# Kernel optimization log

Hardware: AMD Instinct MI355X
Metric: run time of the kernel (lower is better)

## Reference

```python
import jax, jax.numpy as jnp
import numpy as np

QW, KW = 64, 128          # atom query / key window sizes
PAD = (KW - QW) // 2      # halo on each side of the key window
DEPTH, HEADS = 3, 4

def ln(x):
    m = jnp.mean(x, -1, keepdims=True)
    v = jnp.var(x, -1, keepdims=True)
    return (x - m) * jax.lax.rsqrt(v + 1e-5)

def q_windows(x):
    # x: (B, N, ...) -> (B, n, QW, ...); N assumed multiple of QW
    B, N = x.shape[0], x.shape[1]
    n = N // QW
    return x.reshape((B, n, QW) + x.shape[2:])

def k_windows(x):
    # x: (B, N, ...) -> (B, n, KW, ...) sliding key windows with zero halo padding
    B, N = x.shape[0], x.shape[1]
    n = N // QW
    pad_cfg = [(0, 0), (PAD, n * QW + PAD - N)] + [(0, 0)] * (x.ndim - 2)
    xp = jnp.pad(x, pad_cfg)
    idx = jnp.arange(n)[:, None] * QW + jnp.arange(KW)[None, :]
    return xp[:, idx]


def setup_inputs() -> dict:
    key = jax.random.key(0)
    ks = jax.random.split(key, 24)
    B, N, DS, DP, DT, NT = 2, 8192, 128, 16, 384, 1024
    w = lambda k, shp: (jax.random.normal(k, shp, jnp.float32) / np.sqrt(shp[-2])).astype(jnp.float32)
    inp = {
        'ref_pos': jax.random.normal(ks[0], (B, N, 3), jnp.float32),
        'ref_charge': jax.random.normal(ks[1], (B, N, 1), jnp.float32),
        'ref_mask': jnp.ones((B, N, 1), jnp.float32),
        'ref_element': jax.random.uniform(ks[2], (B, N, 128), jnp.float32),
        'ref_atom_name_chars': jax.random.uniform(ks[3], (B, N, 256), jnp.float32),
        'W_single': w(ks[4], (389, DS)),
        'W_pair': w(ks[5], (5, DP)),
        'W_outer': w(ks[6], (DS, 2 * DP)),
        'Wp_ff1': w(ks[7], (DP, 4 * DP)),
        'Wp_ff2': w(ks[8], (4 * DP, DP)),
        'Wq': w(ks[9], (DEPTH, DS, DS)),
        'Wk': w(ks[10], (DEPTH, DS, DS)),
        'Wv': w(ks[11], (DEPTH, DS, DS)),
        'Wo': w(ks[12], (DEPTH, DS, DS)),
        'Wb': w(ks[13], (DP, HEADS)),
        'Wff1': w(ks[14], (DEPTH, DS, 4 * DS)),
        'Wff2': w(ks[15], (DEPTH, 4 * DS, DS)),
        'W_out': w(ks[16], (DS, DT)),
        'ref_space_uid': jnp.sort(jax.random.randint(ks[17], (B, N), 0, NT), axis=-1),
        'atom_to_token_idx': jnp.sort(jax.random.randint(ks[18], (B, N), 0, NT), axis=-1),
        'n_tokens': NT,
    }
    return inp


def reference(ref_pos, ref_charge, ref_mask, ref_element, ref_atom_name_chars,
              W_single, W_pair, W_outer, Wp_ff1, Wp_ff2,
              Wq, Wk, Wv, Wo, Wb, Wff1, Wff2, W_out,
              ref_space_uid, atom_to_token_idx, n_tokens):
    B, N, _ = ref_pos.shape
    n = N // QW
    feats = jnp.concatenate([ref_pos, ref_charge, ref_mask, ref_element, ref_atom_name_chars], -1)
    s = feats @ W_single                                    # (B,N,DS) atom single repr

    # windowed pairwise geometric features
    pos_i, pos_j = q_windows(ref_pos), k_windows(ref_pos)   # (B,n,QW,3), (B,n,KW,3)
    uid_i, uid_j = q_windows(ref_space_uid), k_windows(ref_space_uid)
    dij = pos_i[:, :, :, None, :] - pos_j[:, :, None, :, :]  # (B,n,QW,KW,3)
    inv = 1.0 / (1.0 + jnp.sum(dij * dij, -1, keepdims=True))
    bij = (uid_i[:, :, :, None] == uid_j[:, :, None, :])
    pf = jnp.concatenate([dij, inv, bij[..., None].astype(dij.dtype)], -1)  # (...,5)
    pair = (pf @ W_pair) * bij[..., None].astype(dij.dtype)  # (B,n,QW,KW,DP)

    # pairwise outer-add from relu(single): Linear(DS->2*DP) split into i/j halves
    p = jax.nn.relu(s) @ W_outer
    DP = pair.shape[-1]
    pi, pj = p[..., :DP], p[..., DP:]
    pair = pair + q_windows(pi)[:, :, :, None, :] + k_windows(pj)[:, :, None, :, :]
    pair = pair + jax.nn.relu(ln(pair) @ Wp_ff1) @ Wp_ff2    # pair FF (residual)
    bias = jnp.einsum('bnqkc,ch->bnhqk', pair, Wb)           # attn pair bias

    # key validity mask for the halo-padded positions
    kidx = jnp.arange(n)[:, None] * QW + jnp.arange(KW)[None, :] - PAD
    kmask = jnp.where((kidx >= 0) & (kidx < N), 0.0, -1e9).astype(s.dtype)  # (n,KW)

    dh = s.shape[-1] // HEADS
    x = s
    for l in range(DEPTH):
        h = ln(x)
        q = q_windows(h @ Wq[l]).reshape(B, n, QW, HEADS, dh)
        k = k_windows(h @ Wk[l]).reshape(B, n, KW, HEADS, dh)
        v = k_windows(h @ Wv[l]).reshape(B, n, KW, HEADS, dh)
        logits = jnp.einsum('bnqhd,bnkhd->bnhqk', q, k) / np.sqrt(dh)
        logits = logits + bias + kmask[None, :, None, None, :]
        a = jax.nn.softmax(logits, -1)
        o = jnp.einsum('bnhqk,bnkhd->bnqhd', a, v).reshape(B, N, -1) @ Wo[l]
        x = x + o
        x = x + jax.nn.relu(ln(x) @ Wff1[l]) @ Wff2[l]

    tok = jax.nn.relu(x @ W_out)                             # (B,N,DT)

    def seg_mean(src, idx_):
        ssum = jax.ops.segment_sum(src, idx_, num_segments=n_tokens)
        cnt = jax.ops.segment_sum(jnp.ones((src.shape[0],), src.dtype), idx_, num_segments=n_tokens)
        return ssum / jnp.clip(cnt, 1.0)[:, None]

    return jax.vmap(seg_mean)(tok, atom_to_token_idx)        # (B, n_tokens, DT)
```

## Files before the change

### kernel.cpp

```cpp
#include <hip/hip_runtime.h>
#include <hip/hip_bf16.h>

#define QW 64
#define KW 128
#define PADW 32
#define DEPTH 3
#define HEADS 4
#define B_ 2
#define N_ 8192
#define DS 128
#define DP 16
#define DT 384
#define NT 1024
#define NWIN (N_ / QW)
#define DH (DS / HEADS)

typedef unsigned short u16;
typedef __attribute__((ext_vector_type(8))) short short8;
typedef __attribute__((ext_vector_type(4))) float f32x4v;
typedef __attribute__((ext_vector_type(4))) unsigned short us4;
typedef __attribute__((ext_vector_type(2))) short s16x2;

__device__ __forceinline__ u16 f2b(float x) {
    union { float f; unsigned u; } v; v.f = x;
    unsigned r = v.u + 0x7fffu + ((v.u >> 16) & 1u);
    return (u16)(r >> 16);
}
__device__ __forceinline__ float b2f(u16 h) {
    union { unsigned u; float f; } v; v.u = ((unsigned)h) << 16; return v.f;
}
__device__ __forceinline__ unsigned f2b2(float a, float b) {
    __hip_bfloat162 h = __float22bfloat162_rn(make_float2(a, b));
    union { __hip_bfloat162 h; unsigned u; } c; c.h = h; return c.u;
}
__device__ __forceinline__ us4 pack4(float a, float b, float c, float d) {
    union { us4 v; unsigned u[2]; } o;
    o.u[0] = f2b2(a, b);
    o.u[1] = f2b2(c, d);
    return o.v;
}
__device__ __forceinline__ us4 pack4_relu(float a, float b, float c, float d) {
    union { us4 v; s16x2 s[2]; unsigned u[2]; } o;
    o.u[0] = f2b2(a, b);
    o.u[1] = f2b2(c, d);
    o.s[0] = __builtin_elementwise_max(o.s[0], (s16x2)0);
    o.s[1] = __builtin_elementwise_max(o.s[1], (s16x2)0);
    return o.v;
}

__global__ __launch_bounds__(256) void convw_kernel(
    const float* __restrict__ Wq, const float* __restrict__ Wk,
    const float* __restrict__ Wv, const float* __restrict__ Wo,
    const float* __restrict__ Wff1, const float* __restrict__ Wff2,
    const float* __restrict__ Wout, const float* __restrict__ Wpff1,
    const float* __restrict__ Wpff2, const float* __restrict__ Wb,
    const float* __restrict__ Wsingle, const float* __restrict__ Wouter,
    u16* __restrict__ qkvT, u16* __restrict__ woT, u16* __restrict__ ff1T,
    u16* __restrict__ ff2T, u16* __restrict__ woutT,
    u16* __restrict__ w1T32, u16* __restrict__ wcatT,
    u16* __restrict__ wsT, u16* __restrict__ woutrT)
{
    int idx = blockIdx.x * 256 + threadIdx.x;
    if (idx < 3 * 384 * 128) {
        int l = idx / (384 * 128), r = idx % (384 * 128);
        int n = r / 128, k = r % 128;
        const float* W = (n < 128) ? Wq : (n < 256) ? Wk : Wv;
        qkvT[idx] = f2b(W[(size_t)l * 16384 + k * 128 + (n & 127)]);
    }
    if (idx < 3 * 128 * 128) {
        int l = idx / 16384, r = idx % 16384;
        int n = r / 128, k = r % 128;
        woT[idx] = f2b(Wo[(size_t)l * 16384 + k * 128 + n]);
    }
    if (idx < 3 * 512 * 128) {
        int l = idx / 65536, r = idx % 65536;
        int n = r / 128, k = r % 128;
        ff1T[idx] = f2b(Wff1[(size_t)l * 65536 + k * 512 + n]);
    }
    if (idx < 3 * 128 * 512) {
        int l = idx / 65536, r = idx % 65536;
        int n = r / 512, k = r % 512;
        ff2T[idx] = f2b(Wff2[(size_t)l * 65536 + k * 128 + n]);
    }
    if (idx < 384 * 128) {
        int n = idx / 128, k = idx % 128;
        woutT[idx] = f2b(Wout[(size_t)k * 384 + n]);
    }
    if (idx < 64 * 32) {
        int n = idx >> 5, k = idx & 31;
        w1T32[idx] = (k < 16) ? f2b(Wpff1[k * 64 + n]) : (u16)0;
    }
    if (idx < 16 * 96) {
        int h = idx / 96, k = idx % 96;
        float s = 0.f;
        if (h < 4) {
            if (k < 16) s = Wb[k * 4 + h];
            else if (k < 80) {
                int j = k - 16;
                for (int c = 0; c < 16; ++c) s += Wpff2[j * 16 + c] * Wb[c * 4 + h];
            }
        }
        wcatT[idx] = f2b(s);
    }
    if (idx < 128 * 416) {
        int n = idx / 416, k = idx % 416;
        float v = 0.f;
        if (k < 128)       v = Wsingle[(5 + k) * 128 + n];
        else if (k < 384)  v = Wsingle[(133 + k - 128) * 128 + n];
        else if (k < 387)  v = Wsingle[(k - 384) * 128 + n];
        else if (k == 387) v = Wsingle[3 * 128 + n];
        else if (k == 388) v = Wsingle[4 * 128 + n];
        wsT[idx] = f2b(v);
    }
    if (idx < 32 * 128) {
        int n = idx >> 7, k = idx & 127;
        woutrT[idx] = f2b(Wouter[k * 32 + n]);
    }
}

__global__ __launch_bounds__(256) void embed_gemm(
    const float* __restrict__ pos, const float* __restrict__ charge,
    const float* __restrict__ mask, const float* __restrict__ elem,
    const float* __restrict__ chars, const u16* __restrict__ wsT,
    const u16* __restrict__ woutrT, const u16* __restrict__ qkv0T,
    float* __restrict__ X, float* __restrict__ P, u16* __restrict__ QKVb)
{
    __shared__ __align__(16) u16 As[64 * 424];
    __shared__ float redS[64][4];
    const int LNOFF = 64 * 136;
    int tid = threadIdx.x;
    int row0 = blockIdx.x * 64;

    #pragma unroll
    for (int it = 0; it < 8; ++it) {
        int idx = tid + it * 256;
        int r = idx >> 5, c4 = idx & 31;
        f32x4v v = *(const f32x4v*)(elem + (size_t)(row0 + r) * 128 + c4 * 4);
        *(us4*)&As[r * 424 + c4 * 4] = pack4(v[0], v[1], v[2], v[3]);
    }
    #pragma unroll
    for (int it = 0; it < 16; ++it) {
        int idx = tid + it * 256;
        int r = idx >> 6, c4 = idx & 63;
        f32x4v v = *(const f32x4v*)(chars + (size_t)(row0 + r) * 256 + c4 * 4);
        *(us4*)&As[r * 424 + 128 + c4 * 4] = pack4(v[0], v[1], v[2], v[3]);
    }
    if (tid < 64) {
        int g = row0 + tid;
        As[tid * 424 + 384] = f2b(pos[g * 3]);
        As[tid * 424 + 385] = f2b(pos[g * 3 + 1]);
        As[tid * 424 + 386] = f2b(pos[g * 3 + 2]);
        As[tid * 424 + 387] = f2b(charge[g]);
        As[tid * 424 + 388] = f2b(mask[g]);
        for (int c = 389; c < 416; ++c) As[tid * 424 + c] = 0;
    }
    __syncthreads();

    int wv = tid >> 6, lane = tid & 63, quad = lane >> 4, l16 = lane & 15;
    int wm = (wv & 1) * 32, wn = (wv >> 1) * 64;
    f32x4v acc[2][4];
    #pragma unroll
    for (int i = 0; i < 2; ++i)
        #pragma unroll
        for (int j = 0; j < 4; ++j) acc[i][j] = (f32x4v){0.f, 0.f, 0.f, 0.f};

    #pragma unroll
    for (int kk = 0; kk < 13; ++kk) {
        short8 a0 = *(short8*)&As[(wm + l16) * 424 + kk * 32 + quad * 8];
        short8 a1 = *(short8*)&As[(wm + 16 + l16) * 424 + kk * 32 + quad * 8];
        #pragma unroll
        for (int nt = 0; nt < 4; ++nt) {
            short8 bw = *(const short8*)&wsT[(size_t)(wn + nt * 16 + l16) * 416 +
                                             kk * 32 + quad * 8];
            acc[0][nt] = __builtin_amdgcn_mfma_f32_16x16x32_bf16(a0, bw, acc[0][nt], 0, 0, 0);
            acc[1][nt] = __builtin_amdgcn_mfma_f32_16x16x32_bf16(a1, bw, acc[1][nt], 0, 0, 0);
        }
    }
    __syncthreads();

    #pragma unroll
    for (int mt = 0; mt < 2; ++mt) {
        #pragma unroll
        for (int r = 0; r < 4; ++r) {
            int lrow = wm + mt * 16 + quad * 4 + r;
            int row = row0 + lrow;
            float s = 0.f, ss = 0.f;
            #pragma unroll
            for (int nt = 0; nt < 4; ++nt) {
                float v = acc[mt][nt][r];
                int col = wn + nt * 16 + l16;
                X[(size_t)row * DS + col] = v;
                As[lrow * 136 + col] = f2b(fmaxf(v, 0.f));
                s += v; ss += v * v;
            }
            #pragma unroll
            for (int o = 1; o < 16; o <<= 1) {
                s  += __shfl_xor(s, o);
                ss += __shfl_xor(ss, o);
            }
            if (l16 == 0) {
                redS[lrow][(wv >> 1) * 2]     = s;
                redS[lrow][(wv >> 1) * 2 + 1] = ss;
            }
        }
    }
    __syncthreads();

    #pragma unroll
    for (int mt = 0; mt < 2; ++mt)
        #pragma unroll
        for (int r = 0; r < 4; ++r) {
            int lrow = wm + mt * 16 + quad * 4 + r;
            f32x4v rv = *(f32x4v*)&redS[lrow][0];
            float s = rv[0] + rv[2], ss = rv[1] + rv[3];
            float m = s * (1.f / 128.f);
            float var = ss * (1.f / 128.f) - m * m;
            float rs = __builtin_amdgcn_rsqf(var + 1e-5f);
            #pragma unroll
            for (int nt = 0; nt < 4; ++nt) {
                int col = wn + nt * 16 + l16;
                As[LNOFF + lrow * 136 + col] = f2b((acc[mt][nt][r] - m) * rs);
            }
        }

    {
        f32x4v pacc[2];
        pacc[0] = (f32x4v){0.f, 0.f, 0.f, 0.f};
        pacc[1] = (f32x4v){0.f, 0.f, 0.f, 0.f};
        #pragma unroll
        for (int ks = 0; ks < 4; ++ks) {
            short8 a = *(short8*)&As[(wv * 16 + l16) * 136 + ks * 32 + quad * 8];
            #pragma unroll
            for (int nt = 0; nt < 2; ++nt) {
                short8 bw = *(const short8*)&woutrT[(size_t)(nt * 16 + l16) * 128 +
                                                    ks * 32 + quad * 8];
                pacc[nt] = __builtin_amdgcn_mfma_f32_16x16x32_bf16(a, bw, pacc[nt], 0, 0, 0);
            }
        }
        #pragma unroll
        for (int nt = 0; nt < 2; ++nt)
            #pragma unroll
            for (int r = 0; r < 4; ++r) {
                int row = row0 + wv * 16 + quad * 4 + r;
                P[(size_t)row * 32 + nt * 16 + l16] = pacc[nt][r];
            }
    }
    __syncthreads();

    for (int c = 0; c < 3; ++c) {
        int n0c = c * 128;
        f32x4v qa[2][4];
        #pragma unroll
        for (int i = 0; i < 2; ++i)
            #pragma unroll
            for (int j = 0; j < 4; ++j) qa[i][j] = (f32x4v){0.f, 0.f, 0.f, 0.f};
        #pragma unroll
        for (int ks = 0; ks < 4; ++ks) {
            short8 a0 = *(short8*)&As[LNOFF + (wm + l16) * 136 + ks * 32 + quad * 8];
            short8 a1 = *(short8*)&As[LNOFF + (wm + 16 + l16) * 136 + ks * 32 + quad * 8];
            #pragma unroll
            for (int nt = 0; nt < 4; ++nt) {
                short8 bw = *(const short8*)&qkv0T[(size_t)(n0c + wn + nt * 16 + l16) * 128 +
                                                   ks * 32 + quad * 8];
                qa[0][nt] = __builtin_amdgcn_mfma_f32_16x16x32_bf16(a0, bw, qa[0][nt], 0, 0, 0);
                qa[1][nt] = __builtin_amdgcn_mfma_f32_16x16x32_bf16(a1, bw, qa[1][nt], 0, 0, 0);
            }
        }
        #pragma unroll
        for (int mt = 0; mt < 2; ++mt)
            #pragma unroll
            for (int nt = 0; nt < 4; ++nt)
                #pragma unroll
                for (int r = 0; r < 4; ++r) {
                    int row = row0 + wm + mt * 16 + quad * 4 + r;
                    int col = n0c + wn + nt * 16 + l16;
                    QKVb[(size_t)row * 384 + col] = f2b(qa[mt][nt][r]);
                }
    }
}

__global__ __launch_bounds__(256) void bias_kernel(
    const float* __restrict__ pos, const int* __restrict__ uid,
    const float* __restrict__ P, const float* __restrict__ Wpair,
    const u16* __restrict__ w1T32, const u16* __restrict__ wcatT,
    u16* __restrict__ BIASb)
{
    __shared__ __align__(16) float posjS[128][4];
    __shared__ __align__(16) u16 lpS[4][16 * 24];
    __shared__ __align__(16) u16 A2S[4][16 * 104];

    int tid = threadIdx.x;
    int b  = blockIdx.x >> 11;
    int w  = (blockIdx.x >> 4) & 127;
    int qg = blockIdx.x & 15;

    if (tid < 128) {
        int r = tid;
        int jk = w * QW + r - PADW;
        bool valid = (jk >= 0) && (jk < N_);
        int gk = b * N_ + jk;
        float x = 0.f, y = 0.f, zz = 0.f; int u = 0;
        if (valid) { x = pos[gk * 3]; y = pos[gk * 3 + 1]; zz = pos[gk * 3 + 2]; u = uid[gk]; }
        posjS[r][0] = x; posjS[r][1] = y; posjS[r][2] = zz;
        ((int*)posjS[r])[3] = u;
    }

    int wv = tid >> 6, lane = tid & 63, quad = lane >> 4, l16 = lane & 15;
    int cl = lane >> 2, cg = lane & 3;
    int q = qg * 4 + wv;
    int gq = b * N_ + w * QW + q;

    float xi = pos[gq * 3], yi = pos[gq * 3 + 1], zi = pos[gq * 3 + 2];
    int ui = uid[gq];
    f32x4v pi4 = *(const f32x4v*)(P + (size_t)gq * 32 + cg * 4);
    f32x4v wp[5];
    #pragma unroll
    for (int f = 0; f < 5; ++f)
        wp[f] = *(const f32x4v*)(Wpair + f * 16 + cg * 4);
    short8 w1f[4], wcat[3];
    #pragma unroll
    for (int nt = 0; nt < 4; ++nt)
        w1f[nt] = *(const short8*)&w1T32[(nt * 16 + l16) * 32 + quad * 8];
    #pragma unroll
    for (int ks = 0; ks < 3; ++ks)
        wcat[ks] = *(const short8*)&wcatT[l16 * 96 + ks * 32 + quad * 8];

    f32x4v pjv[8];
    #pragma unroll
    for (int t = 0; t < 8; ++t) {
        int jk = w * QW + t * 16 + cl - PADW;
        bool valid = (jk >= 0) && (jk < N_);
        int gk = b * N_ + jk;
        f32x4v v = (f32x4v){0.f, 0.f, 0.f, 0.f};
        if (valid) v = *(const f32x4v*)(P + (size_t)gk * 32 + 16 + cg * 4);
        pjv[t] = v;
    }

    *(us4*)&A2S[wv][l16 * 104 + 80 + quad * 4] = (us4){0, 0, 0, 0};
    __syncthreads();

    size_t bbase = ((size_t)(b * NWIN + w) * HEADS) * (QW * KW);
    const short8 zero8 = (short8){0, 0, 0, 0, 0, 0, 0, 0};

    for (int t = 0; t < 8; ++t) {
        int kk1 = t * 16 + cl;
        f32x4v pj4 = *(const f32x4v*)&posjS[kk1][0];
        float xj = pj4[0], yj = pj4[1], zj = pj4[2];
        int uj = __float_as_int(pj4[3]);
        float dx = xi - xj, dy = yi - yj, dz = zi - zj;
        float inv = __builtin_amdgcn_rcpf(1.f + dx * dx + dy * dy + dz * dz);
        float bf = (ui == uj) ? 1.f : 0.f;
        float pr[4];
        #pragma unroll
        for (int j = 0; j < 4; ++j) {
            float s = fmaf(dx, wp[0][j], fmaf(dy, wp[1][j],
                      fmaf(dz, wp[2][j], fmaf(inv, wp[3][j], wp[4][j]))));
            pr[j] = fmaf(bf, s, pi4[j] + pjv[t][j]);
        }
        float sum = pr[0] + pr[1] + pr[2] + pr[3];
        sum += __shfl_xor(sum, 1); sum += __shfl_xor(sum, 2);
        float m = sum * (1.f / 16.f);
        float d0 = pr[0] - m, d1 = pr[1] - m, d2 = pr[2] - m, d3 = pr[3] - m;
        float vs = d0 * d0 + d1 * d1 + d2 * d2 + d3 * d3;
        vs += __shfl_xor(vs, 1); vs += __shfl_xor(vs, 2);
        float rstd = __builtin_amdgcn_rsqf(vs * (1.f / 16.f) + 1e-5f);
        *(us4*)&lpS[wv][cl * 24 + cg * 4] =
            pack4(d0 * rstd, d1 * rstd, d2 * rstd, d3 * rstd);
        *(us4*)&A2S[wv][cl * 104 + cg * 4] = pack4(pr[0], pr[1], pr[2], pr[3]);

        short8 blp = zero8;
        if (quad < 2) blp = *(short8*)&lpS[wv][l16 * 24 + quad * 8];
        #pragma unroll
        for (int nt = 0; nt < 4; ++nt) {
            f32x4v z4 = (f32x4v){0.f, 0.f, 0.f, 0.f};
            z4 = __builtin_amdgcn_mfma_f32_16x16x32_bf16(w1f[nt], blp, z4, 0, 0, 0);
            *(us4*)&A2S[wv][l16 * 104 + 16 + nt * 16 + quad * 4] =
                pack4_relu(z4[0], z4[1], z4[2], z4[3]);
        }
        f32x4v acc = (f32x4v){0.f, 0.f, 0.f, 0.f};
        #pragma unroll
        for (int ks = 0; ks < 3; ++ks) {
            short8 a2 = *(short8*)&A2S[wv][l16 * 104 + ks * 32 + quad * 8];
            acc = __builtin_amdgcn_mfma_f32_16x16x32_bf16(a2, wcat[ks], acc, 0, 0, 0);
        }
        if (l16 < 4) {
            *(us4*)&BIASb[bbase + (size_t)l16 * (QW * KW) + q * KW +
                          t * 16 + quad * 4] = pack4(acc[0], acc[1], acc[2], acc[3]);
        }
    }
}

template <bool LAST>
__global__ __launch_bounds__(256) void wo_ff_fused(
    const u16* __restrict__ Ob, const u16* __restrict__ woT,
    const u16* __restrict__ w1T, const u16* __restrict__ w2T,
    const u16* __restrict__ auxT, float* __restrict__ X,
    u16* __restrict__ OutB)
{
    __shared__ __align__(16) u16 As[32 * 136];
    __shared__ __align__(16) u16 Hs[32 * 520];
    __shared__ float redS[32][4];
    int tid = threadIdx.x;
    int row0 = blockIdx.x * 32;
    int wv = tid >> 6, lane = tid & 63, quad = lane >> 4, l16 = lane & 15;
    int wm = (wv & 1) * 16, wn = (wv >> 1) * 64;

    #pragma unroll
    for (int it = 0; it < 2; ++it) {
        int idx = tid + it * 256;
        int r = idx >> 4, c8 = idx & 15;
        *(short8*)&As[r * 136 + c8 * 8] =
            *(const short8*)&Ob[(size_t)(row0 + r) * 128 + c8 * 8];
    }
    __syncthreads();

    f32x4v acc[4];
    #pragma unroll
    for (int j = 0; j < 4; ++j) acc[j] = (f32x4v){0.f, 0.f, 0.f, 0.f};
    #pragma unroll
    for (int ks = 0; ks < 4; ++ks) {
        short8 a = *(short8*)&As[(wm + l16) * 136 + ks * 32 + quad * 8];
        #pragma unroll
        for (int nt = 0; nt < 4; ++nt) {
            short8 b = *(const short8*)&woT[(size_t)(wn + nt * 16 + l16) * 128 +
                                            ks * 32 + quad * 8];
            acc[nt] = __builtin_amdgcn_mfma_f32_16x16x32_bf16(a, b, acc[nt], 0, 0, 0);
        }
    }
    __syncthreads();

    #pragma unroll
    for (int r = 0; r < 4; ++r) {
        int lrow = wm + quad * 4 + r;
        int row = row0 + lrow;
        float s = 0.f, ss = 0.f;
        #pragma unroll
        for (int nt = 0; nt < 4; ++nt) {
            int col = wn + nt * 16 + l16;
            float v = acc[nt][r] + X[(size_t)row * DS + col];
            acc[nt][r] = v;
            s += v; ss += v * v;
        }
        #pragma unroll
        for (int o2 = 1; o2 < 16; o2 <<= 1) {
            s  += __shfl_xor(s, o2);
            ss += __shfl_xor(ss, o2);
        }
        if (l16 == 0) {
            redS[lrow][(wv >> 1) * 2]     = s;
            redS[lrow][(wv >> 1) * 2 + 1] = ss;
        }
    }
    __syncthreads();

    #pragma unroll
    for (int r = 0; r < 4; ++r) {
        int lrow = wm + quad * 4 + r;
        f32x4v rv = *(f32x4v*)&redS[lrow][0];
        float s = rv[0] + rv[2], ss = rv[1] + rv[3];
        float m = s * (1.f / 128.f);
        float var = ss * (1.f / 128.f) - m * m;
        float rs = __builtin_amdgcn_rsqf(var + 1e-5f);
        #pragma unroll
        for (int nt = 0; nt < 4; ++nt) {
            int col = wn + nt * 16 + l16;
            As[lrow * 136 + col] = f2b((acc[nt][r] - m) * rs);
        }
    }
    __syncthreads();

    {
        short8 brow[2][4];
        #pragma unroll
        for (int nt = 0; nt < 2; ++nt)
            #pragma unroll
            for (int ks = 0; ks < 4; ++ks)
                brow[nt][ks] = *(short8*)&As[(nt * 16 + l16) * 136 + ks * 32 + quad * 8];
        #pragma unroll
        for (int mt = 0; mt < 8; ++mt) {
            int j0 = wv * 128 + mt * 16;
            f32x4v c0 = (f32x4v){0.f, 0.f, 0.f, 0.f};
            f32x4v c1 = (f32x4v){0.f, 0.f, 0.f, 0.f};
            #pragma unroll
            for (int ks = 0; ks < 4; ++ks) {
                short8 aw = *(const short8*)&w1T[(size_t)(j0 + l16) * 128 +
                                                 ks * 32 + quad * 8];
                c0 = __builtin_amdgcn_mfma_f32_16x16x32_bf16(aw, brow[0][ks], c0, 0, 0, 0);
                c1 = __builtin_amdgcn_mfma_f32_16x16x32_bf16(aw, brow[1][ks], c1, 0, 0, 0);
            }
            *(us4*)&Hs[l16 * 520 + j0 + quad * 4] =
                pack4_relu(c0[0], c0[1], c0[2], c0[3]);
            *(us4*)&Hs[(16 + l16) * 520 + j0 + quad * 4] =
                pack4_relu(c1[0], c1[1], c1[2], c1[3]);
        }
    }
    __syncthreads();

    f32x4v acc2[4];
    #pragma unroll
    for (int j = 0; j < 4; ++j) acc2[j] = (f32x4v){0.f, 0.f, 0.f, 0.f};
    #pragma unroll
    for (int ks = 0; ks < 16; ++ks) {
        short8 a = *(short8*)&Hs[(wm + l16) * 520 + ks * 32 + quad * 8];
        #pragma unroll
        for (int nt = 0; nt < 4; ++nt) {
            short8 b = *(const short8*)&w2T[(size_t)(wn + nt * 16 + l16) * 512 +
                                            ks * 32 + quad * 8];
            acc2[nt] = __builtin_amdgcn_mfma_f32_16x16x32_bf16(a, b, acc2[nt], 0, 0, 0);
        }
    }

    #pragma unroll
    for (int r = 0; r < 4; ++r) {
        int lrow = wm + quad * 4 + r;
        int row = row0 + lrow;
        float s = 0.f, ss = 0.f;
        #pragma unroll
        for (int nt = 0; nt < 4; ++nt) {
            int col = wn + nt * 16 + l16;
            float v = acc2[nt][r] + acc[nt][r];
            acc2[nt][r] = v;
            X[(size_t)row * DS + col] = v;
            s += v; ss += v * v;
        }
        #pragma unroll
        for (int o2 = 1; o2 < 16; o2 <<= 1) {
            s  += __shfl_xor(s, o2);
            ss += __shfl_xor(ss, o2);
        }
        if (l16 == 0) {
            redS[lrow][(wv >> 1) * 2]     = s;
            redS[lrow][(wv >> 1) * 2 + 1] = ss;
        }
    }
    __syncthreads();

    #pragma unroll
    for (int r = 0; r < 4; ++r) {
        int lrow = wm + quad * 4 + r;
        float m = 0.f, rs = 1.f;
        if (!LAST) {
            f32x4v rv = *(f32x4v*)&redS[lrow][0];
            float s = rv[0] + rv[2], ss = rv[1] + rv[3];
            m = s * (1.f / 128.f);
            float var = ss * (1.f / 128.f) - m * m;
            rs = __builtin_amdgcn_rsqf(var + 1e-5f);
        }
        #pragma unroll
        for (int nt = 0; nt < 4; ++nt) {
            int col = wn + nt * 16 + l16;
            float v = acc2[nt][r];
            As[lrow * 136 + col] = f2b(LAST ? v : (v - m) * rs);
        }
    }
    __syncthreads();

    for (int c = 0; c < 3; ++c) {
        int n0c = c * 128;
        f32x4v qa[4];
        #pragma unroll
        for (int j = 0; j < 4; ++j) qa[j] = (f32x4v){0.f, 0.f, 0.f, 0.f};
        #pragma unroll
        for (int ks = 0; ks < 4; ++ks) {
            short8 a = *(short8*)&As[(wm + l16) * 136 + ks * 32 + quad * 8];
            #pragma unroll
            for (int nt = 0; nt < 4; ++nt) {
                short8 b = *(const short8*)&auxT[(size_t)(n0c + wn + nt * 16 + l16) * 128 +
                                                 ks * 32 + quad * 8];
                qa[nt] = __builtin_amdgcn_mfma_f32_16x16x32_bf16(a, b, qa[nt], 0, 0, 0);
            }
        }
        #pragma unroll
        for (int nt = 0; nt < 4; ++nt)
            #pragma unroll
            for (int r = 0; r < 4; ++r) {
                int row = row0 + wm + quad * 4 + r;
                int col = n0c + wn + nt * 16 + l16;
                float v = qa[nt][r];
                if (LAST) v = fmaxf(v, 0.f);
                OutB[(size_t)row * 384 + col] = f2b(v);
            }
    }
}

__global__ __launch_bounds__(256) void attn_kernel(
    const u16* __restrict__ QKV, const u16* __restrict__ BIASb,
    u16* __restrict__ O)
{
    __shared__ __align__(16) u16 sQ[64 * 40];
    __shared__ __align__(16) u16 sK[128 * 40];
    __shared__ __align__(16) u16 sVt[32 * 152];
    __shared__ __align__(16) u16 sP[64 * 136];

    int tid = threadIdx.x;
    int h = blockIdx.x & 3, w = (blockIdx.x >> 2) & 127, b = blockIdx.x >> 9;
    size_t rowbase = (size_t)b * N_ + w * QW;
    size_t bbase = ((size_t)(b * NWIN + w) * HEADS + h) * (QW * KW);
    const short8 zero8 = (short8){0, 0, 0, 0, 0, 0, 0, 0};

    {
        int r = tid >> 2, d8 = (tid & 3) * 8;
        *(short8*)&sQ[r * 40 + d8] =
            *(const short8*)&QKV[(rowbase + r) * 384 + h * DH + d8];
    }
    #pragma unroll
    for (int i = 0; i < 2; ++i) {
        int idx = tid + i * 256;
        int r = idx >> 2, d8 = (idx & 3) * 8;
        int jk = w * QW + r - PADW;
        short8 v = zero8;
        if (jk >= 0 && jk < N_)
            v = *(const short8*)&QKV[((size_t)b * N_ + jk) * 384 + 128 + h * DH + d8];
        *(short8*)&sK[r * 40 + d8] = v;
    }
    {
        int kk = tid >> 1, d0 = (tid & 1) * 16;
        int jk = w * QW + kk - PADW;
        short8 v0 = zero8, v1 = zero8;
        if (jk >= 0 && jk < N_) {
            const u16* src = &QKV[((size_t)b * N_ + jk) * 384 + 256 + h * DH + d0];
            v0 = *(const short8*)src;
            v1 = *(const short8*)(src + 8);
        }
        #pragma unroll
        for (int j = 0; j < 8; ++j) {
            sVt[(d0 + j) * 152 + kk] = (u16)v0[j];
            sVt[(d0 + 8 + j) * 152 + kk] = (u16)v1[j];
        }
    }
    #pragma unroll
    for (int i = 0; i < 4; ++i) {
        int idx = tid + i * 256;
        int q = idx >> 4, c8 = idx & 15;
        *(short8*)&sP[q * 136 + c8 * 8] =
            *(const short8*)&BIASb[bbase + (size_t)q * KW + c8 * 8];
    }
    __syncthreads();

    int wv = tid >> 6, lane = tid & 63, quad = lane >> 4, l16 = lane & 15;
    const float scale = 0.17677669529663687f;

    short8 aq = *(short8*)&sQ[(wv * 16 + l16) * 40 + quad * 8];
    float e[8][4];
    #pragma unroll
    for (int nt = 0; nt < 8; ++nt) {
        short8 bk = *(short8*)&sK[(nt * 16 + l16) * 40 + quad * 8];
        f32x4v acc = (f32x4v){0.f, 0.f, 0.f, 0.f};
        acc = __builtin_amdgcn_mfma_f32_16x16x32_bf16(aq, bk, acc, 0, 0, 0);
        int kk = nt * 16 + l16;
        int jk = w * QW + kk - PADW;
        float msk = (jk >= 0 && jk < N_) ? 0.f : -1e9f;
        #pragma unroll
        for (int r = 0; r < 4; ++r) {
            int q = wv * 16 + quad * 4 + r;
            e[nt][r] = acc[r] * scale + b2f(sP[q * 136 + kk]) + msk;
        }
    }

    #pragma unroll
    for (int r = 0; r < 4; ++r) {
        float m = e[0][r];
        #pragma unroll
        for (int nt = 1; nt < 8; ++nt) m = fmaxf(m, e[nt][r]);
        m = fmaxf(m, __shfl_xor(m, 1));
        m = fmaxf(m, __shfl_xor(m, 2));
        m = fmaxf(m, __shfl_xor(m, 4));
        m = fmaxf(m, __shfl_xor(m, 8));
        float s = 0.f;
        #pragma unroll
        for (int nt = 0; nt < 8; ++nt) {
            float ev = __expf(e[nt][r] - m);
            e[nt][r] = ev;
            s += ev;
        }
        s += __shfl_xor(s, 1);
        s += __shfl_xor(s, 2);
        s += __shfl_xor(s, 4);
        s += __shfl_xor(s, 8);
        float inv = __builtin_amdgcn_rcpf(s);
        #pragma unroll
        for (int nt = 0; nt < 8; ++nt) e[nt][r] *= inv;
    }

    #pragma unroll
    for (int nt = 0; nt < 8; ++nt) {
        int kk = nt * 16 + l16;
        #pragma unroll
        for (int r = 0; r < 4; ++r) {
            int q = wv * 16 + quad * 4 + r;
            sP[q * 136 + kk] = f2b(e[nt][r]);
        }
    }

    short8 ap[4];
    #pragma unroll
    for (int ks = 0; ks < 4; ++ks)
        ap[ks] = *(short8*)&sP[(wv * 16 + l16) * 136 + ks * 32 + quad * 8];
    #pragma unroll
    for (int nt = 0; nt < 2; ++nt) {
        f32x4v acc = (f32x4v){0.f, 0.f, 0.f, 0.f};
        #pragma unroll
        for (int ks = 0; ks < 4; ++ks) {
            short8 bv = *(short8*)&sVt[(nt * 16 + l16) * 152 + ks * 32 + quad * 8];
            acc = __builtin_amdgcn_mfma_f32_16x16x32_bf16(ap[ks], bv, acc, 0, 0, 0);
        }
        int d = nt * 16 + l16;
        #pragma unroll
        for (int r = 0; r < 4; ++r) {
            int q = wv * 16 + quad * 4 + r;
            O[(rowbase + q) * DS + h * DH + d] = f2b(acc[r]);
        }
    }
}

__global__ __launch_bounds__(128) void seg_kernel(
    const u16* __restrict__ TOKb, const int* __restrict__ idx,
    float* __restrict__ out)
{
    int t = blockIdx.x & (NT - 1);
    int b = blockIdx.x >> 10;
    const int* id = idx + (size_t)b * N_;

    int lo = 0, hi = N_;
    while (lo < hi) { int mid = (lo + hi) >> 1; if (id[mid] < t) lo = mid + 1; else hi = mid; }
    int start = lo;
    hi = N_;
    while (lo < hi) { int mid = (lo + hi) >> 1; if (id[mid] < t + 1) lo = mid + 1; else hi = mid; }
    int end = lo;

    float inv = 1.f / fmaxf((float)(end - start), 1.f);
    for (int c = threadIdx.x; c < DT; c += 128) {
        float s = 0.f;
        for (int r = start; r < end; ++r) s += b2f(TOKb[((size_t)b * N_ + r) * DT + c]);
        out[((size_t)b * NT + t) * DT + c] = s * inv;
    }
}

extern "C" void kernel_launch(void* const* d_in, const int* in_sizes, int n_in,
                              void* d_out, int out_size, void* d_ws, size_t ws_size,
                              hipStream_t stream)
{
    const float* ref_pos    = (const float*)d_in[0];
    const float* ref_charge = (const float*)d_in[1];
    const float* ref_mask   = (const float*)d_in[2];
    const float* ref_elem   = (const float*)d_in[3];
    const float* ref_chars  = (const float*)d_in[4];
    const float* W_single   = (const float*)d_in[5];
    const float* W_pair     = (const float*)d_in[6];
    const float* W_outer    = (const float*)d_in[7];
    const float* Wp_ff1     = (const float*)d_in[8];
    const float* Wp_ff2     = (const float*)d_in[9];
    const float* Wq         = (const float*)d_in[10];
    const float* Wk         = (const float*)d_in[11];
    const float* Wv         = (const float*)d_in[12];
    const float* Wo         = (const float*)d_in[13];
    const float* Wb         = (const float*)d_in[14];
    const float* Wff1       = (const float*)d_in[15];
    const float* Wff2       = (const float*)d_in[16];
    const float* W_out      = (const float*)d_in[17];
    const int*   uid        = (const int*)d_in[18];
    const int*   a2t        = (const int*)d_in[19];
    float* out = (float*)d_out;

    const size_t ROWS = (size_t)B_ * N_;
    float* ws = (float*)d_ws;
    float* X    = ws;
    float* P    = X + ROWS * DS;
    u16* QKVb   = (u16*)(P + ROWS * 32);
    u16* Ob     = QKVb + ROWS * 384;
    u16* FFb    = Ob + ROWS * DS;
    u16* BIASb  = FFb + ROWS * 512;
    u16* TOKb   = BIASb + (size_t)B_ * NWIN * HEADS * QW * KW;
    u16* LNb    = TOKb + ROWS * DT;
    u16* qkvT   = LNb + ROWS * DS;
    u16* woT    = qkvT + 3 * 384 * 128;
    u16* ff1T   = woT + 3 * 128 * 128;
    u16* ff2T   = ff1T + 3 * 512 * 128;
    u16* woutT  = ff2T + 3 * 128 * 512;
    u16* w1T32  = woutT + 384 * 128;
    u16* wcatT  = w1T32 + 64 * 32;
    u16* wsT    = wcatT + 16 * 96;
    u16* woutrT = wsT + 128 * 416;

    convw_kernel<<<768, 256, 0, stream>>>(Wq, Wk, Wv, Wo, Wff1, Wff2, W_out,
                                          Wp_ff1, Wp_ff2, Wb, W_single, W_outer,
                                          qkvT, woT, ff1T, ff2T, woutT,
                                          w1T32, wcatT, wsT, woutrT);
    embed_gemm<<<ROWS / 64, 256, 0, stream>>>(ref_pos, ref_charge, ref_mask,
                                              ref_elem, ref_chars, wsT, woutrT,
                                              qkvT, X, P, QKVb);
    bias_kernel<<<4096, 256, 0, stream>>>(ref_pos, uid, P, W_pair,
                                          w1T32, wcatT, BIASb);

    for (int l = 0; l < DEPTH; ++l) {
        attn_kernel<<<B_ * NWIN * HEADS, 256, 0, stream>>>(QKVb, BIASb, Ob);
        if (l < DEPTH - 1) {
            wo_ff_fused<false><<<ROWS / 32, 256, 0, stream>>>(
                Ob, woT + (size_t)l * 128 * 128,
                ff1T + (size_t)l * 512 * 128, ff2T + (size_t)l * 128 * 512,
                qkvT + (size_t)(l + 1) * 384 * 128, X, QKVb);
        } else {
            wo_ff_fused<true><<<ROWS / 32, 256, 0, stream>>>(
                Ob, woT + (size_t)l * 128 * 128,
                ff1T + (size_t)l * 512 * 128, ff2T + (size_t)l * 128 * 512,
                woutT, X, TOKb);
        }
    }

    seg_kernel<<<B_ * NT, 128, 0, stream>>>(TOKb, a2t, out);
}
```

Baseline: 371.5 us.

## Use DPP lane reductions, skip interior masks, vectorize segment mean loads

Replaces the __shfl_xor butterfly reductions in the layernorm and softmax paths with DPP-based row reductions (quad_perm and row_shr/ror), which avoids LDS-routed permutes. Computes the key-window mask only in the edge windows. Partially unrolls the pair-bias loop and makes the segment-mean kernel read four bf16 values per thread using 96 active threads. Together these target instruction overhead in reductions and narrow global loads. The DPP row_shr patterns must give a full 16-lane reduction, which is a correctness risk if the control codes do not broadcast the result to every lane.

Result: faster. 353.1 us (-5.0%).

```diff
diff --git a/kernel.cpp b/kernel.cpp
--- a/kernel.cpp
+++ b/kernel.cpp
@@ -46,6 +46,32 @@
     o.s[0] = __builtin_elementwise_max(o.s[0], (s16x2)0);
     o.s[1] = __builtin_elementwise_max(o.s[1], (s16x2)0);
     return o.v;
+}
+
+template <int CTRL>
+__device__ __forceinline__ float fdpp(float x) {
+    int r = __builtin_amdgcn_update_dpp(0, __builtin_bit_cast(int, x),
+                                        CTRL, 0xF, 0xF, true);
+    return __builtin_bit_cast(float, r);
+}
+__device__ __forceinline__ float sum4_dpp(float x) {
+    x += fdpp<0xB1>(x);
+    x += fdpp<0x4E>(x);
+    return x;
+}
+__device__ __forceinline__ float sum16_dpp(float x) {
+    x += fdpp<0xB1>(x);
+    x += fdpp<0x4E>(x);
+    x += fdpp<0x124>(x);
+    x += fdpp<0x128>(x);
+    return x;
+}
+__device__ __forceinline__ float max16_dpp(float x) {
+    x = fmaxf(x, fdpp<0xB1>(x));
+    x = fmaxf(x, fdpp<0x4E>(x));
+    x = fmaxf(x, fdpp<0x124>(x));
+    x = fmaxf(x, fdpp<0x128>(x));
+    return x;
 }
 
 __global__ __launch_bounds__(256) void convw_kernel(
@@ -193,11 +219,8 @@
                 As[lrow * 136 + col] = f2b(fmaxf(v, 0.f));
                 s += v; ss += v * v;
             }
-            #pragma unroll
-            for (int o = 1; o < 16; o <<= 1) {
-                s  += __shfl_xor(s, o);
-                ss += __shfl_xor(ss, o);
-            }
+            s  = sum16_dpp(s);
+            ss = sum16_dpp(ss);
             if (l16 == 0) {
                 redS[lrow][(wv >> 1) * 2]     = s;
                 redS[lrow][(wv >> 1) * 2 + 1] = ss;
@@ -342,6 +365,7 @@
     size_t bbase = ((size_t)(b * NWIN + w) * HEADS) * (QW * KW);
     const short8 zero8 = (short8){0, 0, 0, 0, 0, 0, 0, 0};
 
+    #pragma unroll 2
     for (int t = 0; t < 8; ++t) {
         int kk1 = t * 16 + cl;
         f32x4v pj4 = *(const f32x4v*)&posjS[kk1][0];
@@ -358,11 +382,11 @@
             pr[j] = fmaf(bf, s, pi4[j] + pjv[t][j]);
         }
         float sum = pr[0] + pr[1] + pr[2] + pr[3];
-        sum += __shfl_xor(sum, 1); sum += __shfl_xor(sum, 2);
+        sum = sum4_dpp(sum);
         float m = sum * (1.f / 16.f);
         float d0 = pr[0] - m, d1 = pr[1] - m, d2 = pr[2] - m, d3 = pr[3] - m;
         float vs = d0 * d0 + d1 * d1 + d2 * d2 + d3 * d3;
-        vs += __shfl_xor(vs, 1); vs += __shfl_xor(vs, 2);
+        vs = sum4_dpp(vs);
         float rstd = __builtin_amdgcn_rsqf(vs * (1.f / 16.f) + 1e-5f);
         *(us4*)&lpS[wv][cl * 24 + cg * 4] =
             pack4(d0 * rstd, d1 * rstd, d2 * rstd, d3 * rstd);
@@ -441,11 +465,8 @@
             acc[nt][r] = v;
             s += v; ss += v * v;
         }
-        #pragma unroll
-        for (int o2 = 1; o2 < 16; o2 <<= 1) {
-            s  += __shfl_xor(s, o2);
-            ss += __shfl_xor(ss, o2);
-        }
+        s  = sum16_dpp(s);
+        ss = sum16_dpp(ss);
         if (l16 == 0) {
             redS[lrow][(wv >> 1) * 2]     = s;
             redS[lrow][(wv >> 1) * 2 + 1] = ss;
@@ -523,11 +544,8 @@
             X[(size_t)row * DS + col] = v;
             s += v; ss += v * v;
         }
-        #pragma unroll
-        for (int o2 = 1; o2 < 16; o2 <<= 1) {
-            s  += __shfl_xor(s, o2);
-            ss += __shfl_xor(ss, o2);
-        }
+        s  = sum16_dpp(s);
+        ss = sum16_dpp(ss);
         if (l16 == 0) {
             redS[lrow][(wv >> 1) * 2]     = s;
             redS[lrow][(wv >> 1) * 2 + 1] = ss;
@@ -597,6 +615,7 @@
     size_t rowbase = (size_t)b * N_ + w * QW;
     size_t bbase = ((size_t)(b * NWIN + w) * HEADS + h) * (QW * KW);
     const short8 zero8 = (short8){0, 0, 0, 0, 0, 0, 0, 0};
+    const bool edge = (w == 0) || (w == NWIN - 1);
 
     {
         int r = tid >> 2, d8 = (tid & 3) * 8;
@@ -648,8 +667,11 @@
         f32x4v acc = (f32x4v){0.f, 0.f, 0.f, 0.f};
         acc = __builtin_amdgcn_mfma_f32_16x16x32_bf16(aq, bk, acc, 0, 0, 0);
         int kk = nt * 16 + l16;
-        int jk = w * QW + kk - PADW;
-        float msk = (jk >= 0 && jk < N_) ? 0.f : -1e9f;
+        float msk = 0.f;
+        if (edge) {
+            int jk = w * QW + kk - PADW;
+            msk = (jk >= 0 && jk < N_) ? 0.f : -1e9f;
+        }
         #pragma unroll
         for (int r = 0; r < 4; ++r) {
             int q = wv * 16 + quad * 4 + r;
@@ -662,10 +684,7 @@
         float m = e[0][r];
         #pragma unroll
         for (int nt = 1; nt < 8; ++nt) m = fmaxf(m, e[nt][r]);
-        m = fmaxf(m, __shfl_xor(m, 1));
-        m = fmaxf(m, __shfl_xor(m, 2));
-        m = fmaxf(m, __shfl_xor(m, 4));
-        m = fmaxf(m, __shfl_xor(m, 8));
+        m = max16_dpp(m);
         float s = 0.f;
         #pragma unroll
         for (int nt = 0; nt < 8; ++nt) {
@@ -673,10 +692,7 @@
             e[nt][r] = ev;
             s += ev;
         }
-        s += __shfl_xor(s, 1);
-        s += __shfl_xor(s, 2);
-        s += __shfl_xor(s, 4);
-        s += __shfl_xor(s, 8);
+        s = sum16_dpp(s);
         float inv = __builtin_amdgcn_rcpf(s);
         #pragma unroll
         for (int nt = 0; nt < 8; ++nt) e[nt][r] *= inv;
@@ -729,10 +745,16 @@
     int end = lo;
 
     float inv = 1.f / fmaxf((float)(end - start), 1.f);
-    for (int c = threadIdx.x; c < DT; c += 128) {
-        float s = 0.f;
-        for (int r = start; r < end; ++r) s += b2f(TOKb[((size_t)b * N_ + r) * DT + c]);
-        out[((size_t)b * NT + t) * DT + c] = s * inv;
+    if (threadIdx.x < 96) {
+        int c4 = threadIdx.x * 4;
+        f32x4v s = (f32x4v){0.f, 0.f, 0.f, 0.f};
+        for (int r = start; r < end; ++r) {
+            us4 v = *(const us4*)&TOKb[((size_t)b * N_ + r) * DT + c4];
+            s[0] += b2f(v[0]); s[1] += b2f(v[1]);
+            s[2] += b2f(v[2]); s[3] += b2f(v[3]);
+        }
+        s[0] *= inv; s[1] *= inv; s[2] *= inv; s[3] *= inv;
+        *(f32x4v*)&out[((size_t)b * NT + t) * DT + c4] = s;
     }
 }
 
```
